# Kernel optimization log

Hardware: AMD Instinct MI355X
Metric: run time of the kernel (lower is better)

The kernel has to match this reference:

```python
import jax, jax.numpy as jnp
import numpy as np

KY, KX = 3, 3  # kernel_size from init_kwargs


def setup_inputs() -> dict:
    key = jax.random.key(0)
    x = jax.random.normal(key, (8, 32, 512, 512), dtype=jnp.float32)
    return {"x": x}


def reference(x):
    # Replicate-pad H by (KY-1)//2, W by (KX-1)//2 (matches F.pad mode='replicate').
    py, px = (KY - 1) // 2, (KX - 1) // 2
    B, C, H, W = x.shape
    padded = jnp.pad(x, ((0, 0), (0, 0), (py, py), (px, px)), mode='edge')
    center = (KY * KX) // 2
    # The torch module builds an identity neigh2channel kernel with the center
    # tap zeroed, then maxes over the KY*KX channels. The zeroed center channel
    # contributes a constant 0 to that max, so we initialize the running max at 0
    # and fold in every non-center neighbor via shifted slices (no blown-up
    # [B,C,KY*KX,H,W] tensor is materialized).
    m = jnp.zeros_like(x)
    for idx in range(KY * KX):
        if idx == center:
            continue
        i, j = divmod(idx, KX)
        m = jnp.maximum(m, padded[:, :, i:i + H, j:j + W])
    mask = (x > m).astype(x.dtype)
    return x * mask
```

## Files before the change

### kernel.cpp

```cpp
#include <hip/hip_runtime.h>


#define IMG_W 512
#define IMG_H 512
#define RPT 8
#define THREADS 256

__device__ __forceinline__ float4 vmax4(float4 a, float4 b) {
    return make_float4(fmaxf(a.x, b.x), fmaxf(a.y, b.y),
                       fmaxf(a.z, b.z), fmaxf(a.w, b.w));
}

__global__ __launch_bounds__(THREADS)
void nms3x3_kernel(const float* __restrict__ x, float* __restrict__ out) {
    const int cg   = threadIdx.x & 127;
    const int half = threadIdx.x >> 7;
    const int c0   = cg << 2;
    const int r0   = blockIdx.x * (2 * RPT) + half * RPT;
    const size_t plane = (size_t)blockIdx.y * IMG_H * IMG_W;
    const float* img  = x + plane;
    float*       oimg = out + plane;

    const int cl = (c0 == 0) ? 0 : c0 - 1;
    const int cr = (c0 + 4 >= IMG_W) ? IMG_W - 1 : c0 + 4;

    auto loadrow = [&](int r, float4& h3o, float4& h2o, float4& vo) {
        r = min(IMG_H - 1, max(0, r));
        const float* rowp = img + (size_t)r * IMG_W;
        const float4 v  = *(const float4*)(rowp + c0);
        const float  sL = rowp[cl];
        const float  sR = rowp[cr];
        const float4 l  = make_float4(sL, v.x, v.y, v.z);
        const float4 rr = make_float4(v.y, v.z, v.w, sR);
        h2o = vmax4(l, rr);
        h3o = vmax4(h2o, v);
        vo  = v;
    };

    float4 h3p, h2p, vp, h3c, h2c, vc, h3n, h2n, vn;
    loadrow(r0 - 1, h3p, h2p, vp);
    loadrow(r0,     h3c, h2c, vc);

#pragma unroll
    for (int k = 0; k < RPT; ++k) {
        loadrow(r0 + k + 1, h3n, h2n, vn);
        float4 m8 = vmax4(vmax4(h3p, h3n), h2c);
        float4 o;
        o.x = (vc.x > fmaxf(m8.x, 0.0f)) ? vc.x : 0.0f;
        o.y = (vc.y > fmaxf(m8.y, 0.0f)) ? vc.y : 0.0f;
        o.z = (vc.z > fmaxf(m8.z, 0.0f)) ? vc.z : 0.0f;
        o.w = (vc.w > fmaxf(m8.w, 0.0f)) ? vc.w : 0.0f;
        *(float4*)(oimg + (size_t)(r0 + k) * IMG_W + c0) = o;
        h3p = h3c; h2p = h2c; vp = vc;
        h3c = h3n; h2c = h2n; vc = vn;
    }
}

extern "C" void kernel_launch(void* const* d_in, const int* in_sizes, int n_in,
                              void* d_out, int out_size, void* d_ws, size_t ws_size,
                              hipStream_t stream) {
    const float* x = (const float*)d_in[0];
    float* out     = (float*)d_out;
    dim3 grid(IMG_H / (2 * RPT), 8 * 32);
    nms3x3_kernel<<<grid, dim3(THREADS), 0, stream>>>(x, out);
}
```

Before: 426.9 us.

## Map full rows to one wave with shuffle halos and taller row strips

Each wavefront now owns an entire 512-wide row, as two float4 column chunks per lane, and processes 32 rows instead of 8. Horizontal neighbor values come from cross-lane shuffles instead of extra scalar global loads. The taller strip shrinks the share of halo rows that are loaded twice. In exchange there are fewer blocks (1024 vs 8192), more registers per thread, and extra shuffle instructions, which may reduce memory-level parallelism and occupancy.

```diff
diff --git a/kernel.cpp b/kernel.cpp
--- a/kernel.cpp
+++ b/kernel.cpp
@@ -3,56 +3,74 @@
 
 #define IMG_W 512
 #define IMG_H 512
-#define RPT 8
-#define THREADS 256
+#define RPT 32
+#define WAVES 4
+#define THREADS (WAVES * 64)
+#define BLOCK_ROWS (WAVES * RPT)
 
 __device__ __forceinline__ float4 vmax4(float4 a, float4 b) {
     return make_float4(fmaxf(a.x, b.x), fmaxf(a.y, b.y),
                        fmaxf(a.z, b.z), fmaxf(a.w, b.w));
 }
 
+struct RowState { float4 h3A, h2A, vA, h3B, h2B, vB; };
+
 __global__ __launch_bounds__(THREADS)
 void nms3x3_kernel(const float* __restrict__ x, float* __restrict__ out) {
-    const int cg   = threadIdx.x & 127;
-    const int half = threadIdx.x >> 7;
-    const int c0   = cg << 2;
-    const int r0   = blockIdx.x * (2 * RPT) + half * RPT;
+    const int lane = threadIdx.x & 63;
+    const int wave = threadIdx.x >> 6;
+    const int r0   = blockIdx.x * BLOCK_ROWS + wave * RPT;
     const size_t plane = (size_t)blockIdx.y * IMG_H * IMG_W;
     const float* img  = x + plane;
     float*       oimg = out + plane;
+    const int cA = lane << 2;
+    const int cB = 256 + (lane << 2);
 
-    const int cl = (c0 == 0) ? 0 : c0 - 1;
-    const int cr = (c0 + 4 >= IMG_W) ? IMG_W - 1 : c0 + 4;
-
-    auto loadrow = [&](int r, float4& h3o, float4& h2o, float4& vo) {
+    auto loadrow = [&](int r, RowState& o) {
         r = min(IMG_H - 1, max(0, r));
         const float* rowp = img + (size_t)r * IMG_W;
-        const float4 v  = *(const float4*)(rowp + c0);
-        const float  sL = rowp[cl];
-        const float  sR = rowp[cr];
-        const float4 l  = make_float4(sL, v.x, v.y, v.z);
-        const float4 rr = make_float4(v.y, v.z, v.w, sR);
-        h2o = vmax4(l, rr);
-        h3o = vmax4(h2o, v);
-        vo  = v;
+        const float4 vA = *(const float4*)(rowp + cA);
+        const float4 vB = *(const float4*)(rowp + cB);
+        const float aw_l = __shfl_up(vA.w, 1);
+        const float ax_r = __shfl_down(vA.x, 1);
+        const float bw_l = __shfl_up(vB.w, 1);
+        const float bx_r = __shfl_down(vB.x, 1);
+        const float aw63 = __shfl(vA.w, 63);
+        const float bx0  = __shfl(vB.x, 0);
+        const float sLA = (lane == 0)  ? vA.x : aw_l;
+        const float sRA = (lane == 63) ? bx0  : ax_r;
+        const float sLB = (lane == 0)  ? aw63 : bw_l;
+        const float sRB = (lane == 63) ? vB.w : bx_r;
+        const float4 lA = make_float4(sLA, vA.x, vA.y, vA.z);
+        const float4 rA = make_float4(vA.y, vA.z, vA.w, sRA);
+        o.h2A = vmax4(lA, rA); o.h3A = vmax4(o.h2A, vA); o.vA = vA;
+        const float4 lB = make_float4(sLB, vB.x, vB.y, vB.z);
+        const float4 rB = make_float4(vB.y, vB.z, vB.w, sRB);
+        o.h2B = vmax4(lB, rB); o.h3B = vmax4(o.h2B, vB); o.vB = vB;
     };
 
-    float4 h3p, h2p, vp, h3c, h2c, vc, h3n, h2n, vn;
-    loadrow(r0 - 1, h3p, h2p, vp);
-    loadrow(r0,     h3c, h2c, vc);
+    RowState p, c, n;
+    loadrow(r0 - 1, p);
+    loadrow(r0,     c);
 
-#pragma unroll
+#pragma unroll 8
     for (int k = 0; k < RPT; ++k) {
-        loadrow(r0 + k + 1, h3n, h2n, vn);
-        float4 m8 = vmax4(vmax4(h3p, h3n), h2c);
-        float4 o;
-        o.x = (vc.x > fmaxf(m8.x, 0.0f)) ? vc.x : 0.0f;
-        o.y = (vc.y > fmaxf(m8.y, 0.0f)) ? vc.y : 0.0f;
-        o.z = (vc.z > fmaxf(m8.z, 0.0f)) ? vc.z : 0.0f;
-        o.w = (vc.w > fmaxf(m8.w, 0.0f)) ? vc.w : 0.0f;
-        *(float4*)(oimg + (size_t)(r0 + k) * IMG_W + c0) = o;
-        h3p = h3c; h2p = h2c; vp = vc;
-        h3c = h3n; h2c = h2n; vc = vn;
+        loadrow(r0 + k + 1, n);
+        const float4 mA = vmax4(vmax4(p.h3A, n.h3A), c.h2A);
+        const float4 mB = vmax4(vmax4(p.h3B, n.h3B), c.h2B);
+        float4 oA, oB;
+        oA.x = (c.vA.x > fmaxf(mA.x, 0.0f)) ? c.vA.x : 0.0f;
+        oA.y = (c.vA.y > fmaxf(mA.y, 0.0f)) ? c.vA.y : 0.0f;
+        oA.z = (c.vA.z > fmaxf(mA.z, 0.0f)) ? c.vA.z : 0.0f;
+        oA.w = (c.vA.w > fmaxf(mA.w, 0.0f)) ? c.vA.w : 0.0f;
+        oB.x = (c.vB.x > fmaxf(mB.x, 0.0f)) ? c.vB.x : 0.0f;
+        oB.y = (c.vB.y > fmaxf(mB.y, 0.0f)) ? c.vB.y : 0.0f;
+        oB.z = (c.vB.z > fmaxf(mB.z, 0.0f)) ? c.vB.z : 0.0f;
+        oB.w = (c.vB.w > fmaxf(mB.w, 0.0f)) ? c.vB.w : 0.0f;
+        float* orow = oimg + (size_t)(r0 + k) * IMG_W;
+        *(float4*)(orow + cA) = oA;
+        *(float4*)(orow + cB) = oB;
+        p = c; c = n;
     }
 }
 
@@ -61,6 +79,6 @@
                               hipStream_t stream) {
     const float* x = (const float*)d_in[0];
     float* out     = (float*)d_out;
-    dim3 grid(IMG_H / (2 * RPT), 8 * 32);
+    dim3 grid(IMG_H / BLOCK_ROWS, 8 * 32);
     nms3x3_kernel<<<grid, dim3(THREADS), 0, stream>>>(x, out);
 }
```

After: 443.2 us. 3.8% more time.
